# Kernel optimization log

Hardware: AMD Instinct MI355X
Metric: run time of the kernel (lower is better)

## Reference

```python
import jax, jax.numpy as jnp
import numpy as np

D_MODEL = 1024
N_HEADS = 16
D_HEAD = D_MODEL // N_HEADS
B, S = 4, 2048


def setup_inputs() -> dict:
    key = jax.random.key(0)
    ks = jax.random.split(key, 12)
    std = 1.0 / np.sqrt(D_MODEL)
    inp = {
        "q": jax.random.normal(ks[0], (B, S, D_MODEL), jnp.float32),
        "k": jax.random.normal(ks[1], (B, S, D_MODEL), jnp.float32),
        "v": jax.random.normal(ks[2], (B, S, D_MODEL), jnp.float32),
        # causal mask: 1 where attention is disallowed (j > i)
        "mask": jnp.triu(jnp.ones((S, S), jnp.int32), k=1)[None, None],
        "Wq": jax.random.normal(ks[3], (D_MODEL, D_MODEL), jnp.float32) * std,
        "bq": jnp.zeros((D_MODEL,), jnp.float32),
        "Wk": jax.random.normal(ks[4], (D_MODEL, D_MODEL), jnp.float32) * std,
        "bk": jnp.zeros((D_MODEL,), jnp.float32),
        "Wv": jax.random.normal(ks[5], (D_MODEL, D_MODEL), jnp.float32) * std,
        "bv": jnp.zeros((D_MODEL,), jnp.float32),
        "Wo": jax.random.normal(ks[6], (D_MODEL, D_MODEL), jnp.float32) * std,
        "bo": jnp.zeros((D_MODEL,), jnp.float32),
    }
    return inp


def _split_heads(x):
    # [B, S, D] -> [B, H, S, d_head]
    b, s, _ = x.shape
    return x.reshape(b, s, N_HEADS, D_HEAD).transpose(0, 2, 1, 3)


def reference(q, k, v, mask, Wq, bq, Wk, bk, Wv, bv, Wo, bo):
    # torch Linear: y = x @ W.T + b
    qh = _split_heads(q @ Wq.T + bq)
    kh = _split_heads(k @ Wk.T + bk)
    vh = _split_heads(v @ Wv.T + bv)
    # NOTE: original scales by sqrt(d_model), not sqrt(d_head)
    scale = 1.0 / np.sqrt(D_MODEL).astype(np.float32)
    logits = jnp.einsum("bhqd,bhkd->bhqk", qh, kh) * scale
    logits = logits + mask.astype(logits.dtype) * (-1e9)
    weights = jax.nn.softmax(logits, axis=-1)
    attn = jnp.einsum("bhqk,bhkd->bhqd", weights, vh)
    attn = attn.transpose(0, 2, 1, 3).reshape(q.shape[0], -1, D_MODEL)
    out = attn @ Wo.T + bo
    return out, weights
```

## Files before the change

### kernel.cpp

```cpp
#include <hip/hip_runtime.h>
#include <stdint.h>

typedef unsigned short u16;
typedef __attribute__((ext_vector_type(8))) short bf16x8;
typedef __attribute__((ext_vector_type(8))) unsigned short us8;
typedef __attribute__((ext_vector_type(4))) float f32x4;

typedef __attribute__((address_space(1))) void as1_void;
typedef __attribute__((address_space(3))) void as3_void;

#define S_LEN 2048
#define DMODEL 1024
#define DH 64
#define NHEADS 16
#define NB 4
#define GM (NB * S_LEN)
#define GN DMODEL
#define GK DMODEL
#define SCALE 0.03125f

__device__ __forceinline__ void gload16(const void* g, void* l) {
  __builtin_amdgcn_global_load_lds((const as1_void*)g, (as3_void*)l, 16, 0, 0);
}
__device__ __forceinline__ float bf2f(u16 u) {
  union { unsigned int i; float f; } x; x.i = ((unsigned int)u) << 16; return x.f;
}
__device__ __forceinline__ u16 f2bf(float f) {
  union { float f; unsigned int i; } x; x.f = f;
  unsigned int u = x.i + 0x7fffu + ((x.i >> 16) & 1u);
  return (u16)(u >> 16);
}
__device__ __forceinline__ f32x4 mfma16(bf16x8 a, bf16x8 b, f32x4 c) {
  return __builtin_amdgcn_mfma_f32_16x16x32_bf16(a, b, c, 0, 0, 0);
}
__device__ __forceinline__ void nt_store4(f32x4 v, float* p) {
  __builtin_nontemporal_store(v, (f32x4*)p);
}

__device__ __forceinline__ void cvt_chunk(const float* s, u16* d, int i) {
  const f32x4 a = *(const f32x4*)(s + (size_t)i * 8);
  const f32x4 b = *(const f32x4*)(s + (size_t)i * 8 + 4);
  us8 o;
  o[0] = f2bf(a[0]); o[1] = f2bf(a[1]); o[2] = f2bf(a[2]); o[3] = f2bf(a[3]);
  o[4] = f2bf(b[0]); o[5] = f2bf(b[1]); o[6] = f2bf(b[2]); o[7] = f2bf(b[3]);
  *(us8*)(d + (size_t)i * 8) = o;
}
__global__ __launch_bounds__(256)
void cvt3(const float* __restrict__ s0, const float* __restrict__ s1,
          const float* __restrict__ s2, u16* __restrict__ d0,
          u16* __restrict__ d1, u16* __restrict__ d2, int n8) {
  const int i = blockIdx.x * 256 + threadIdx.x;
  if (i >= n8) return;
  const float* s; u16* d;
  if (blockIdx.y == 0)      { s = s0; d = d0; }
  else if (blockIdx.y == 1) { s = s1; d = d1; }
  else                      { s = s2; d = d2; }
  cvt_chunk(s, d, i);
}
__global__ __launch_bounds__(256)
void cvt4(const float* __restrict__ s0, const float* __restrict__ s1,
          const float* __restrict__ s2, const float* __restrict__ s3,
          u16* __restrict__ d0, u16* __restrict__ d1,
          u16* __restrict__ d2, u16* __restrict__ d3, int n8) {
  const int i = blockIdx.x * 256 + threadIdx.x;
  if (i >= n8) return;
  const float* s; u16* d;
  if (blockIdx.y == 0)      { s = s0; d = d0; }
  else if (blockIdx.y == 1) { s = s1; d = d1; }
  else if (blockIdx.y == 2) { s = s2; d = d2; }
  else                      { s = s3; d = d3; }
  cvt_chunk(s, d, i);
}

template<bool OUTF>
__device__ __forceinline__ void gemm_body(const u16* __restrict__ A,
                                          const u16* __restrict__ W,
                                          const float* __restrict__ bias,
                                          void* __restrict__ Cv,
                                          u16* smem) {
  u16* As = smem;
  u16* Bs = smem + 2 * 8192;
  const int tid  = threadIdx.x;
  const int lane = tid & 63;
  const int wv   = tid >> 6;
  const int wr   = wv >> 1, wc = wv & 1;
  const int rlow = lane & 15, rhi = lane >> 4;
  const int m0 = blockIdx.x * 128;
  const int n0 = blockIdx.y * 128;

  f32x4 acc[4][4];
#pragma unroll
  for (int i = 0; i < 4; ++i)
#pragma unroll
    for (int j = 0; j < 4; ++j) acc[i][j] = (f32x4){0.f, 0.f, 0.f, 0.f};

#define STAGE_G(bufi, kk)                                                     \
  {                                                                           \
    _Pragma("unroll")                                                         \
    for (int i = 0; i < 4; ++i) {                                             \
      const int c = i * 256 + tid;                                            \
      const int row = c >> 3, cw = c & 7;                                     \
      const int koff = ((kk) << 6) + ((cw ^ (row & 7)) << 3);                 \
      gload16(A + (size_t)(m0 + row) * GK + koff,                             \
              &As[(bufi) * 8192 + ((c - lane) << 3)]);                        \
      gload16(W + (size_t)(n0 + row) * GK + koff,                             \
              &Bs[(bufi) * 8192 + ((c - lane) << 3)]);                        \
    }                                                                         \
  }

  const int nk = GK >> 6;
  STAGE_G(0, 0);
  __syncthreads();
  int buf = 0;
  for (int kk = 0; kk < nk; ++kk) {
    if (kk + 1 < nk) STAGE_G(buf ^ 1, kk + 1);
    const u16* Ab = &As[buf * 8192];
    const u16* Bb = &Bs[buf * 8192];
    bf16x8 af[4][2], bfr[4][2];
#pragma unroll
    for (int mi = 0; mi < 4; ++mi) {
      const int row = wr * 64 + mi * 16 + rlow;
#pragma unroll
      for (int k2 = 0; k2 < 2; ++k2)
        af[mi][k2] = *(const bf16x8*)&Ab[row * 64 + (((rhi + k2 * 4) ^ (row & 7)) << 3)];
    }
#pragma unroll
    for (int ni = 0; ni < 4; ++ni) {
      const int row = wc * 64 + ni * 16 + rlow;
#pragma unroll
      for (int k2 = 0; k2 < 2; ++k2)
        bfr[ni][k2] = *(const bf16x8*)&Bb[row * 64 + (((rhi + k2 * 4) ^ (row & 7)) << 3)];
    }
#pragma unroll
    for (int mi = 0; mi < 4; ++mi)
#pragma unroll
      for (int ni = 0; ni < 4; ++ni) {
        acc[mi][ni] = mfma16(af[mi][0], bfr[ni][0], acc[mi][ni]);
        acc[mi][ni] = mfma16(af[mi][1], bfr[ni][1], acc[mi][ni]);
      }
    __syncthreads();
    buf ^= 1;
  }
#undef STAGE_G

  if constexpr (OUTF) {
    float* Cs = (float*)smem;
#pragma unroll
    for (int ni = 0; ni < 4; ++ni) {
      const int col = wc * 64 + ni * 16 + rlow;
      const float bv = bias[n0 + col];
#pragma unroll
      for (int mi = 0; mi < 4; ++mi)
#pragma unroll
        for (int r = 0; r < 4; ++r)
          Cs[(wr * 64 + mi * 16 + rhi * 4 + r) * 128 + col] = acc[mi][ni][r] + bv;
    }
    __syncthreads();
#pragma unroll
    for (int i = 0; i < 16; ++i) {
      const int c = i * 256 + tid;
      const int row = c >> 5, cw = c & 31;
      const f32x4 t = *(const f32x4*)&Cs[row * 128 + cw * 4];
      nt_store4(t, &((float*)Cv)[(size_t)(m0 + row) * GN + n0 + cw * 4]);
    }
  } else {
    u16* Cs = smem;
#pragma unroll
    for (int ni = 0; ni < 4; ++ni) {
      const int col = wc * 64 + ni * 16 + rlow;
      const float bv = bias[n0 + col];
#pragma unroll
      for (int mi = 0; mi < 4; ++mi)
#pragma unroll
        for (int r = 0; r < 4; ++r)
          Cs[(wr * 64 + mi * 16 + rhi * 4 + r) * 144 + col] = f2bf(acc[mi][ni][r] + bv);
    }
    __syncthreads();
#pragma unroll
    for (int i = 0; i < 8; ++i) {
      const int c = i * 256 + tid;
      const int row = c >> 4, cw = c & 15;
      const us8 t = *(const us8*)&Cs[row * 144 + cw * 8];
      *(us8*)&((u16*)Cv)[(size_t)(m0 + row) * GN + n0 + cw * 8] = t;
    }
  }
}

__global__ __launch_bounds__(256, 2)
void gemm_qkv(const u16* __restrict__ xq, const u16* __restrict__ xk,
              const u16* __restrict__ xv, const u16* __restrict__ wq,
              const u16* __restrict__ wk, const u16* __restrict__ wv,
              const float* __restrict__ bq, const float* __restrict__ bk,
              const float* __restrict__ bv, u16* __restrict__ oq,
              u16* __restrict__ ok, u16* __restrict__ ov) {
  __shared__ u16 smem[4 * 8192];
  const u16 *A, *W; const float* bias; u16* C;
  if (blockIdx.z == 0)      { A = xq; W = wq; bias = bq; C = oq; }
  else if (blockIdx.z == 1) { A = xk; W = wk; bias = bk; C = ok; }
  else                      { A = xv; W = wv; bias = bv; C = ov; }
  gemm_body<false>(A, W, bias, C, smem);
}

__global__ __launch_bounds__(256, 2)
void gemm_o(const u16* __restrict__ A, const u16* __restrict__ W,
            const float* __restrict__ bias, float* __restrict__ C) {
  __shared__ u16 smem[4 * 8192];
  gemm_body<true>(A, W, bias, C, smem);
}

__global__ __launch_bounds__(512, 4)
void attn_fused(const u16* __restrict__ qh, const u16* __restrict__ kh,
                const u16* __restrict__ vh, float* __restrict__ wout,
                u16* __restrict__ am)
{
  __shared__ u16 smem[34304];
  u16* Ws  = smem;
  u16* Qs  = smem;
  u16* Kb1 = smem;
  u16* Kb0 = smem + 17408;
  u16* VT  = smem + 17408 + 8192;

  const int tid = threadIdx.x, lane = tid & 63, wv = tid >> 6;
  const int rlow = lane & 15, rhi = lane >> 4;
  const int idx = blockIdx.x;
  const int bh  = idx & 63;
  const int qt  = 15 - (idx >> 6);
  const int b = bh >> 4, h = bh & 15;
  const int q0 = qt << 7;
  const size_t headoff = (size_t)b * S_LEN * DMODEL + h * DH;

#define STAGE_K(dst, jtile)                                                   \
  {                                                                           \
    _Pragma("unroll")                                                         \
    for (int i = 0; i < 2; ++i) {                                             \
      const int c = i * 512 + tid;                                            \
      const int row = c >> 3, cw = c & 7;                                     \
      gload16(kh + headoff + (size_t)((jtile) * 128 + row) * DMODEL +         \
              ((cw ^ (row & 7)) << 3), &(dst)[(c - lane) << 3]);              \
    }                                                                         \
  }
#define LOAD_V(jtile)                                                         \
  {                                                                           \
    const int d0v = wv << 3;                                                  \
    vvA = *(const bf16x8*)(vh + headoff +                                     \
          (size_t)((jtile) * 128 + lane) * DMODEL + d0v);                     \
    vvB = *(const bf16x8*)(vh + headoff +                                     \
          (size_t)((jtile) * 128 + 64 + lane) * DMODEL + d0v);                \
  }

#pragma unroll
  for (int i = 0; i < 2; ++i) {
    const int c = i * 512 + tid;
    const int row = c >> 3, cw = c & 7;
    gload16(qh + headoff + (size_t)(q0 + row) * DMODEL + ((cw ^ (row & 7)) << 3),
            &Qs[(c - lane) << 3]);
  }
  __syncthreads();
  bf16x8 qf[2];
  {
    const int row = wv * 16 + rlow;
#pragma unroll
    for (int k2 = 0; k2 < 2; ++k2)
      qf[k2] = *(const bf16x8*)&Qs[row * 64 + (((rhi + k2 * 4) ^ (row & 7)) << 3)];
  }

  const int gi_base = q0 + wv * 16 + rhi * 4;
  float ssum[4] = {0.f, 0.f, 0.f, 0.f};

  STAGE_K(Kb0, 0);
  for (int jt = 0; jt <= qt; ++jt) {
    __syncthreads();
    const u16* kcur = (jt & 1) ? Kb1 : Kb0;
    if (jt < qt) {
      u16* knxt = (jt & 1) ? Kb0 : Kb1;
      STAGE_K(knxt, jt + 1);
    }
    const bool diag = (jt == qt);
    float pexp[4] = {0.f, 0.f, 0.f, 0.f};
#pragma unroll
    for (int half = 0; half < 2; ++half) {
      f32x4 acc[4];
#pragma unroll
      for (int ni = 0; ni < 4; ++ni) acc[ni] = (f32x4){0.f, 0.f, 0.f, 0.f};
#pragma unroll
      for (int k2 = 0; k2 < 2; ++k2) {
#pragma unroll
        for (int ni = 0; ni < 4; ++ni) {
          const int row = (half * 4 + ni) * 16 + rlow;
          bf16x8 kf = *(const bf16x8*)&kcur[row * 64 + (((rhi + k2 * 4) ^ (row & 7)) << 3)];
          acc[ni] = mfma16(qf[k2], kf, acc[ni]);
        }
      }
#pragma unroll
      for (int ni = 0; ni < 4; ++ni) {
        const int gj = jt * 128 + (half * 4 + ni) * 16 + rlow;
#pragma unroll
        for (int r = 0; r < 4; ++r) {
          if (!diag || gj <= gi_base + r) pexp[r] += __expf(acc[ni][r] * SCALE);
        }
      }
    }
#pragma unroll
    for (int r = 0; r < 4; ++r) {
      float p = pexp[r];
      p += __shfl_xor(p, 1);
      p += __shfl_xor(p, 2);
      p += __shfl_xor(p, 4);
      p += __shfl_xor(p, 8);
      ssum[r] += p;
    }
  }
  float inv_s[4];
#pragma unroll
  for (int r = 0; r < 4; ++r) inv_s[r] = 1.f / ssum[r];

  f32x4 opv[4];
#pragma unroll
  for (int ni = 0; ni < 4; ++ni) opv[ni] = (f32x4){0.f, 0.f, 0.f, 0.f};

  bf16x8 vvA, vvB;
  __syncthreads();
  STAGE_K(Kb0, 0);
  LOAD_V(0);
  __syncthreads();

  for (int jt = 0; jt <= qt; ++jt) {
    {
      const int d0v = wv << 3;
#pragma unroll
      for (int e = 0; e < 8; ++e) {
        VT[(d0v + e) * 136 + lane] = (u16)vvA[e];
        VT[(d0v + e) * 136 + 64 + lane] = (u16)vvB[e];
      }
    }
    const bool diag = (jt == qt);
#pragma unroll
    for (int half = 0; half < 2; ++half) {
      f32x4 acc[4];
#pragma unroll
      for (int ni = 0; ni < 4; ++ni) acc[ni] = (f32x4){0.f, 0.f, 0.f, 0.f};
#pragma unroll
      for (int k2 = 0; k2 < 2; ++k2) {
#pragma unroll
        for (int ni = 0; ni < 4; ++ni) {
          const int row = (half * 4 + ni) * 16 + rlow;
          bf16x8 kf = *(const bf16x8*)&Kb0[row * 64 + (((rhi + k2 * 4) ^ (row & 7)) << 3)];
          acc[ni] = mfma16(qf[k2], kf, acc[ni]);
        }
      }
#pragma unroll
      for (int ni = 0; ni < 4; ++ni) {
        const int col = (half * 4 + ni) * 16 + rlow;
        const int gj = jt * 128 + col;
#pragma unroll
        for (int r = 0; r < 4; ++r) {
          float w = 0.f;
          if (!diag || gj <= gi_base + r) w = __expf(acc[ni][r] * SCALE) * inv_s[r];
          Ws[(wv * 16 + rhi * 4 + r) * 136 + col] = f2bf(w);
        }
      }
    }
    __syncthreads();
    if (jt < qt) {
      STAGE_K(Kb0, jt + 1);
      LOAD_V(jt + 1);
    }
    {
      const size_t wbase = ((size_t)bh * S_LEN + q0) * S_LEN + (size_t)jt * 128;
#pragma unroll
      for (int i = 0; i < 8; ++i) {
        const int c = i * 512 + tid;
        const int row = c >> 5, cw = c & 31;
        f32x4 t;
        t[0] = bf2f(Ws[row * 136 + cw * 4 + 0]);
        t[1] = bf2f(Ws[row * 136 + cw * 4 + 1]);
        t[2] = bf2f(Ws[row * 136 + cw * 4 + 2]);
        t[3] = bf2f(Ws[row * 136 + cw * 4 + 3]);
        nt_store4(t, wout + wbase + (size_t)row * S_LEN + cw * 4);
      }
    }
#pragma unroll
    for (int k4 = 0; k4 < 4; ++k4) {
      const bf16x8 afr = *(const bf16x8*)&Ws[(wv * 16 + rlow) * 136 + rhi * 8 + k4 * 32];
#pragma unroll
      for (int ni = 0; ni < 4; ++ni) {
        const bf16x8 vfr = *(const bf16x8*)&VT[(ni * 16 + rlow) * 136 + rhi * 8 + k4 * 32];
        opv[ni] = mfma16(afr, vfr, opv[ni]);
      }
    }
    __syncthreads();
  }
#undef STAGE_K
#undef LOAD_V

  {
    const f32x4 z = {0.f, 0.f, 0.f, 0.f};
    for (int jt = qt + 1; jt < 16; ++jt) {
      const size_t wbase = ((size_t)bh * S_LEN + q0) * S_LEN + (size_t)jt * 128;
#pragma unroll
      for (int i = 0; i < 8; ++i) {
        const int c = i * 512 + tid;
        const int row = c >> 5, cw = c & 31;
        nt_store4(z, wout + wbase + (size_t)row * S_LEN + cw * 4);
      }
    }
  }

  {
    u16* Os = smem;
#pragma unroll
    for (int ni = 0; ni < 4; ++ni)
#pragma unroll
      for (int r = 0; r < 4; ++r)
        Os[(wv * 16 + rhi * 4 + r) * 72 + ni * 16 + rlow] = f2bf(opv[ni][r]);
    __syncthreads();
#pragma unroll
    for (int i = 0; i < 2; ++i) {
      const int c = i * 512 + tid;
      const int row = c >> 3, cw = c & 7;
      const us8 t = *(const us8*)&Os[row * 72 + cw * 8];
      *(us8*)(am + headoff + (size_t)(q0 + row) * DMODEL + cw * 8) = t;
    }
  }
}

extern "C" void kernel_launch(void* const* d_in, const int* in_sizes, int n_in,
                              void* d_out, int out_size, void* d_ws, size_t ws_size,
                              hipStream_t stream) {
  const float* q  = (const float*)d_in[0];
  const float* k  = (const float*)d_in[1];
  const float* v  = (const float*)d_in[2];
  const float* Wq = (const float*)d_in[4];
  const float* bq = (const float*)d_in[5];
  const float* Wk = (const float*)d_in[6];
  const float* bk = (const float*)d_in[7];
  const float* Wv = (const float*)d_in[8];
  const float* bv = (const float*)d_in[9];
  const float* Wo = (const float*)d_in[10];
  const float* bo = (const float*)d_in[11];

  const size_t proj_elems = (size_t)NB * S_LEN * DMODEL;
  const size_t w_elems    = (size_t)DMODEL * DMODEL;
  float* out0 = (float*)d_out;
  float* wts  = out0 + proj_elems;

  u16* qh  = (u16*)d_ws;
  u16* kh  = qh + proj_elems;
  u16* vh  = kh + proj_elems;
  u16* am  = vh + proj_elems;
  u16* wco = am + proj_elems;

  u16* xq = (u16*)wts;
  u16* xk = xq + proj_elems;
  u16* xv = xk + proj_elems;
  u16* wq_ = xv + proj_elems;
  u16* wk_ = wq_ + w_elems;
  u16* wv_ = wk_ + w_elems;

  const int n8x = (int)(proj_elems / 8);
  const int n8w = (int)(w_elems / 8);

  cvt3<<<dim3(n8x / 256, 3), dim3(256), 0, stream>>>(q, k, v, xq, xk, xv, n8x);
  cvt4<<<dim3(n8w / 256, 4), dim3(256), 0, stream>>>(Wq, Wk, Wv, Wo,
                                                     wq_, wk_, wv_, wco, n8w);
  gemm_qkv<<<dim3(64, 8, 3), dim3(256), 0, stream>>>(xq, xk, xv, wq_, wk_, wv_,
                                                     bq, bk, bv, qh, kh, vh);
  attn_fused<<<dim3(1024), dim3(512), 0, stream>>>(qh, kh, vh, wts, am);
  gemm_o<<<dim3(64, 8), dim3(256), 0, stream>>>(am, wco, bo, out0);
}
```

Before: 351.3 us.

## Single-buffer QKV GEMM LDS to raise occupancy to three blocks per CU

The QKV projection GEMM drops double-buffered LDS staging in favour of a single buffer that is loaded, synchronised and consumed each k-step, which halves its shared memory to 32 KB. The launch bound rises to three blocks per CU so more waves can hide latency. The price is that global-to-LDS loads no longer overlap the MFMA work inside a block. The epilogue staging pitch also changes from 144 to 128, which may bring LDS bank conflicts back on the bf16 writeback.

```diff
diff --git a/kernel.cpp b/kernel.cpp
--- a/kernel.cpp
+++ b/kernel.cpp
@@ -72,19 +72,110 @@
   cvt_chunk(s, d, i);
 }
 
-template<bool OUTF>
-__device__ __forceinline__ void gemm_body(const u16* __restrict__ A,
-                                          const u16* __restrict__ W,
-                                          const float* __restrict__ bias,
-                                          void* __restrict__ Cv,
-                                          u16* smem) {
+#define GEMM_IDX                                                              \
+  const int tid  = threadIdx.x;                                               \
+  const int lane = tid & 63;                                                  \
+  const int wvi  = tid >> 6;                                                  \
+  const int wr   = wvi >> 1, wc = wvi & 1;                                    \
+  const int rlow = lane & 15, rhi = lane >> 4;
+
+#define GEMM_COMPUTE(Ab, Bb)                                                  \
+  {                                                                           \
+    bf16x8 af[4][2], bfr[4][2];                                               \
+    _Pragma("unroll")                                                         \
+    for (int mi = 0; mi < 4; ++mi) {                                          \
+      const int row = wr * 64 + mi * 16 + rlow;                               \
+      _Pragma("unroll")                                                       \
+      for (int k2 = 0; k2 < 2; ++k2)                                          \
+        af[mi][k2] = *(const bf16x8*)&(Ab)[row * 64 +                         \
+                     (((rhi + k2 * 4) ^ (row & 7)) << 3)];                    \
+    }                                                                         \
+    _Pragma("unroll")                                                         \
+    for (int ni = 0; ni < 4; ++ni) {                                          \
+      const int row = wc * 64 + ni * 16 + rlow;                               \
+      _Pragma("unroll")                                                       \
+      for (int k2 = 0; k2 < 2; ++k2)                                          \
+        bfr[ni][k2] = *(const bf16x8*)&(Bb)[row * 64 +                        \
+                      (((rhi + k2 * 4) ^ (row & 7)) << 3)];                   \
+    }                                                                         \
+    _Pragma("unroll")                                                         \
+    for (int mi = 0; mi < 4; ++mi)                                            \
+      _Pragma("unroll")                                                       \
+      for (int ni = 0; ni < 4; ++ni) {                                        \
+        acc[mi][ni] = mfma16(af[mi][0], bfr[ni][0], acc[mi][ni]);             \
+        acc[mi][ni] = mfma16(af[mi][1], bfr[ni][1], acc[mi][ni]);             \
+      }                                                                       \
+  }
+
+__global__ __launch_bounds__(256, 3)
+void gemm_qkv(const u16* __restrict__ xq, const u16* __restrict__ xk,
+              const u16* __restrict__ xv, const u16* __restrict__ wq,
+              const u16* __restrict__ wk, const u16* __restrict__ wv,
+              const float* __restrict__ bq, const float* __restrict__ bk,
+              const float* __restrict__ bv, u16* __restrict__ oq,
+              u16* __restrict__ ok, u16* __restrict__ ov) {
+  __shared__ u16 smem[2 * 8192];
+  u16* As = smem;
+  u16* Bs = smem + 8192;
+  const u16 *A, *W; const float* bias; u16* C;
+  if (blockIdx.z == 0)      { A = xq; W = wq; bias = bq; C = oq; }
+  else if (blockIdx.z == 1) { A = xk; W = wk; bias = bk; C = ok; }
+  else                      { A = xv; W = wv; bias = bv; C = ov; }
+  GEMM_IDX
+  const int m0 = blockIdx.x * 128;
+  const int n0 = blockIdx.y * 128;
+
+  f32x4 acc[4][4];
+#pragma unroll
+  for (int i = 0; i < 4; ++i)
+#pragma unroll
+    for (int j = 0; j < 4; ++j) acc[i][j] = (f32x4){0.f, 0.f, 0.f, 0.f};
+
+  const int nk = GK >> 6;
+  for (int kk = 0; kk < nk; ++kk) {
+#pragma unroll
+    for (int i = 0; i < 4; ++i) {
+      const int c = i * 256 + tid;
+      const int row = c >> 3, cw = c & 7;
+      const int koff = (kk << 6) + ((cw ^ (row & 7)) << 3);
+      gload16(A + (size_t)(m0 + row) * GK + koff, &As[(c - lane) << 3]);
+      gload16(W + (size_t)(n0 + row) * GK + koff, &Bs[(c - lane) << 3]);
+    }
+    __syncthreads();
+    GEMM_COMPUTE(As, Bs)
+    __syncthreads();
+  }
+
+  {
+    u16* Cs = smem;
+#pragma unroll
+    for (int ni = 0; ni < 4; ++ni) {
+      const int col = wc * 64 + ni * 16 + rlow;
+      const float bv2 = bias[n0 + col];
+#pragma unroll
+      for (int mi = 0; mi < 4; ++mi)
+#pragma unroll
+        for (int r = 0; r < 4; ++r)
+          Cs[(wr * 64 + mi * 16 + rhi * 4 + r) * 128 + col] = f2bf(acc[mi][ni][r] + bv2);
+    }
+    __syncthreads();
+#pragma unroll
+    for (int i = 0; i < 8; ++i) {
+      const int c = i * 256 + tid;
+      const int row = c >> 4, cw = c & 15;
+      const us8 t = *(const us8*)&Cs[row * 128 + cw * 8];
+      *(us8*)&C[(size_t)(m0 + row) * GN + n0 + cw * 8] = t;
+    }
+  }
+}
+
+__global__ __launch_bounds__(256, 2)
+void gemm_o(const u16* __restrict__ A, const u16* __restrict__ W,
+            const float* __restrict__ bias, float* __restrict__ C) {
+  __shared__ u16 smem[4 * 8192];
   u16* As = smem;
   u16* Bs = smem + 2 * 8192;
-  const int tid  = threadIdx.x;
-  const int lane = tid & 63;
-  const int wv   = tid >> 6;
-  const int wr   = wv >> 1, wc = wv & 1;
-  const int rlow = lane & 15, rhi = lane >> 4;
+  GEMM_IDX
   const int m0 = blockIdx.x * 128;
   const int n0 = blockIdx.y * 128;
 
@@ -116,44 +207,23 @@
     if (kk + 1 < nk) STAGE_G(buf ^ 1, kk + 1);
     const u16* Ab = &As[buf * 8192];
     const u16* Bb = &Bs[buf * 8192];
-    bf16x8 af[4][2], bfr[4][2];
-#pragma unroll
-    for (int mi = 0; mi < 4; ++mi) {
-      const int row = wr * 64 + mi * 16 + rlow;
-#pragma unroll
-      for (int k2 = 0; k2 < 2; ++k2)
-        af[mi][k2] = *(const bf16x8*)&Ab[row * 64 + (((rhi + k2 * 4) ^ (row & 7)) << 3)];
-    }
-#pragma unroll
-    for (int ni = 0; ni < 4; ++ni) {
-      const int row = wc * 64 + ni * 16 + rlow;
-#pragma unroll
-      for (int k2 = 0; k2 < 2; ++k2)
-        bfr[ni][k2] = *(const bf16x8*)&Bb[row * 64 + (((rhi + k2 * 4) ^ (row & 7)) << 3)];
-    }
-#pragma unroll
-    for (int mi = 0; mi < 4; ++mi)
-#pragma unroll
-      for (int ni = 0; ni < 4; ++ni) {
-        acc[mi][ni] = mfma16(af[mi][0], bfr[ni][0], acc[mi][ni]);
-        acc[mi][ni] = mfma16(af[mi][1], bfr[ni][1], acc[mi][ni]);
-      }
+    GEMM_COMPUTE(Ab, Bb)
     __syncthreads();
     buf ^= 1;
   }
 #undef STAGE_G
 
-  if constexpr (OUTF) {
+  {
     float* Cs = (float*)smem;
 #pragma unroll
     for (int ni = 0; ni < 4; ++ni) {
       const int col = wc * 64 + ni * 16 + rlow;
-      const float bv = bias[n0 + col];
+      const float bv2 = bias[n0 + col];
 #pragma unroll
       for (int mi = 0; mi < 4; ++mi)
 #pragma unroll
         for (int r = 0; r < 4; ++r)
-          Cs[(wr * 64 + mi * 16 + rhi * 4 + r) * 128 + col] = acc[mi][ni][r] + bv;
+          Cs[(wr * 64 + mi * 16 + rhi * 4 + r) * 128 + col] = acc[mi][ni][r] + bv2;
     }
     __syncthreads();
 #pragma unroll
@@ -161,51 +231,9 @@
       const int c = i * 256 + tid;
       const int row = c >> 5, cw = c & 31;
       const f32x4 t = *(const f32x4*)&Cs[row * 128 + cw * 4];
-      nt_store4(t, &((float*)Cv)[(size_t)(m0 + row) * GN + n0 + cw * 4]);
-    }
-  } else {
-    u16* Cs = smem;
-#pragma unroll
-    for (int ni = 0; ni < 4; ++ni) {
-      const int col = wc * 64 + ni * 16 + rlow;
-      const float bv = bias[n0 + col];
-#pragma unroll
-      for (int mi = 0; mi < 4; ++mi)
-#pragma unroll
-        for (int r = 0; r < 4; ++r)
-          Cs[(wr * 64 + mi * 16 + rhi * 4 + r) * 144 + col] = f2bf(acc[mi][ni][r] + bv);
-    }
-    __syncthreads();
-#pragma unroll
-    for (int i = 0; i < 8; ++i) {
-      const int c = i * 256 + tid;
-      const int row = c >> 4, cw = c & 15;
-      const us8 t = *(const us8*)&Cs[row * 144 + cw * 8];
-      *(us8*)&((u16*)Cv)[(size_t)(m0 + row) * GN + n0 + cw * 8] = t;
-    }
-  }
-}
-
-__global__ __launch_bounds__(256, 2)
-void gemm_qkv(const u16* __restrict__ xq, const u16* __restrict__ xk,
-              const u16* __restrict__ xv, const u16* __restrict__ wq,
-              const u16* __restrict__ wk, const u16* __restrict__ wv,
-              const float* __restrict__ bq, const float* __restrict__ bk,
-              const float* __restrict__ bv, u16* __restrict__ oq,
-              u16* __restrict__ ok, u16* __restrict__ ov) {
-  __shared__ u16 smem[4 * 8192];
-  const u16 *A, *W; const float* bias; u16* C;
-  if (blockIdx.z == 0)      { A = xq; W = wq; bias = bq; C = oq; }
-  else if (blockIdx.z == 1) { A = xk; W = wk; bias = bk; C = ok; }
-  else                      { A = xv; W = wv; bias = bv; C = ov; }
-  gemm_body<false>(A, W, bias, C, smem);
-}
-
-__global__ __launch_bounds__(256, 2)
-void gemm_o(const u16* __restrict__ A, const u16* __restrict__ W,
-            const float* __restrict__ bias, float* __restrict__ C) {
-  __shared__ u16 smem[4 * 8192];
-  gemm_body<true>(A, W, bias, C, smem);
+      nt_store4(t, &C[(size_t)(m0 + row) * GN + n0 + cw * 4]);
+    }
+  }
 }
 
 __global__ __launch_bounds__(512, 4)
```

Result: no change. 348.3 us (-0.9%).
